# Kernel optimization log

Hardware: AMD Instinct MI355X
Metric: run time of the kernel (lower is better)

The kernel has to match this reference:

```python
import jax, jax.numpy as jnp
import numpy as np

D_MODEL = 512
NUM_HEADS = 8
DEPTH = D_MODEL // NUM_HEADS


def setup_inputs() -> dict:
    key = jax.random.key(0)
    kx, kq, kk, kv, ko = jax.random.split(key, 5)
    scale = 1.0 / np.sqrt(D_MODEL)
    return {
        "x": jax.random.normal(kx, (4, 2048, D_MODEL), dtype=jnp.float32),
        "W_q": jax.random.normal(kq, (D_MODEL, D_MODEL), dtype=jnp.float32) * scale,
        "W_k": jax.random.normal(kk, (D_MODEL, D_MODEL), dtype=jnp.float32) * scale,
        "W_v": jax.random.normal(kv, (D_MODEL, D_MODEL), dtype=jnp.float32) * scale,
        "W_o": jax.random.normal(ko, (D_MODEL, D_MODEL), dtype=jnp.float32) * scale,
    }


def reference(x, W_q, W_k, W_v, W_o):
    B, S, _ = x.shape
    # nn.Linear with weight W: y = x @ W.T
    def split_heads(t):
        return t.reshape(B, S, NUM_HEADS, DEPTH).transpose(0, 2, 1, 3)  # [B,H,S,D]
    Q = split_heads(x @ W_q.T)
    K = split_heads(x @ W_k.T)
    V = split_heads(x @ W_v.T)
    b = -jnp.log(jnp.asarray(S, dtype=jnp.float32))  # -log(seq_len) bias
    inv_sqrt_dk = 1.0 / jnp.sqrt(jnp.asarray(DEPTH, dtype=jnp.float32))
    qk = jnp.einsum('bhqd,bhkd->bhqk', Q, K) * inv_sqrt_dk
    attn = jax.nn.sigmoid(qk + b)  # non-softmax sigmoid attention
    out = jnp.einsum('bhqk,bhkd->bhqd', attn, V)
    out = out.transpose(0, 2, 1, 3).reshape(B, S, D_MODEL)
    return out @ W_o.T
```

## Files before the change

kernel.cpp:

```cpp
#include <hip/hip_runtime.h>
#include <stdint.h>

typedef _Float16 f16x8 __attribute__((ext_vector_type(8)));
typedef _Float16 f16x4 __attribute__((ext_vector_type(4)));
typedef __fp16 h16x2 __attribute__((ext_vector_type(2)));
typedef float f32x4 __attribute__((ext_vector_type(4)));
typedef float f32x16 __attribute__((ext_vector_type(16)));

#define SEQ 2048
#define NHEADS 8

#define GLOAD_LDS16(gp, lp)                                                        \
  __builtin_amdgcn_global_load_lds(                                                \
      (const __attribute__((address_space(1))) void*)(uintptr_t)(const void*)(gp), \
      (__attribute__((address_space(3))) void*)(uintptr_t)(void*)(lp), 16, 0, 0)

__device__ __forceinline__ void barrier_lds() {
  __builtin_amdgcn_s_waitcnt(0xc07f);
  __builtin_amdgcn_s_barrier();
}

__device__ __forceinline__ f16x4 pack4(float a, float b, float c, float d) {
  h16x2 lo = __builtin_amdgcn_cvt_pkrtz(a, b);
  h16x2 hi = __builtin_amdgcn_cvt_pkrtz(c, d);
  f16x4 o;
  o.x = (_Float16)lo.x; o.y = (_Float16)lo.y;
  o.z = (_Float16)hi.x; o.w = (_Float16)hi.y;
  return o;
}

__global__ void cvt_all_kernel(const float* __restrict__ x, const float* __restrict__ wq,
                               const float* __restrict__ wk, const float* __restrict__ wv,
                               const float* __restrict__ wo, _Float16* __restrict__ xh,
                               _Float16* __restrict__ wh) {
  int i = blockIdx.x * 256 + threadIdx.x;
  const float* src;
  _Float16* dst;
  int off;
  if (i < 1048576) {
    src = x; dst = xh; off = i;
  } else {
    int j = i - 1048576;
    int sel = j >> 16;
    off = j & 65535;
    src = (sel == 0) ? wq : (sel == 1) ? wk : (sel == 2) ? wv : wo;
    dst = wh + (size_t)sel * 262144;
  }
  float4 v = ((const float4*)src)[off];
  ((f16x4*)dst)[off] = pack4(v.x, v.y, v.z, v.w);
}

__device__ __forceinline__ void gemm_tile_bt(const _Float16* __restrict__ A,
                                             const _Float16* __restrict__ B,
                                             int m0, int n0,
                                             _Float16* lds,
                                             f32x4 (&acc)[4][4]) {
  const int tid = threadIdx.x;
  const int w = tid >> 6, lane = tid & 63;
  const int wr = w >> 1, wc = w & 1;
  const int lrow = lane & 15, q = lane >> 4;
  const int snb = w * 32 + (lane >> 3);
  const int scb = lane & 7;

#pragma unroll
  for (int i = 0; i < 4; ++i)
#pragma unroll
    for (int j = 0; j < 4; ++j)
#pragma unroll
      for (int r = 0; r < 4; ++r) acc[i][j][r] = 0.f;

#pragma unroll
  for (int t = 0; t < 4; ++t) {
    int n = snb + t * 8;
    int cbg = scb ^ (n & 7);
    GLOAD_LDS16(A + (size_t)(m0 + n) * 512 + cbg * 8, lds + (w * 32 + t * 8) * 64);
    GLOAD_LDS16(B + (size_t)(n0 + n) * 512 + cbg * 8, lds + 8192 + (w * 32 + t * 8) * 64);
  }

  for (int kt = 0; kt < 8; ++kt) {
    __syncthreads();
    if (kt < 7) {
      _Float16* nb = lds + ((kt + 1) & 1) * 16384;
#pragma unroll
      for (int t = 0; t < 4; ++t) {
        int n = snb + t * 8;
        int cbg = scb ^ (n & 7);
        GLOAD_LDS16(A + (size_t)(m0 + n) * 512 + (kt + 1) * 64 + cbg * 8, nb + (w * 32 + t * 8) * 64);
        GLOAD_LDS16(B + (size_t)(n0 + n) * 512 + (kt + 1) * 64 + cbg * 8, nb + 8192 + (w * 32 + t * 8) * 64);
      }
    }
    _Float16* As = lds + (kt & 1) * 16384;
    _Float16* Bs = As + 8192;

    f16x8 af[4][2], bfr[4][2];
#pragma unroll
    for (int i = 0; i < 4; ++i) {
      int m = wr * 64 + i * 16 + lrow;
#pragma unroll
      for (int kk = 0; kk < 2; ++kk) {
        int cb = (kk * 4 + q) ^ (m & 7);
        af[i][kk] = *(const f16x8*)(As + m * 64 + cb * 8);
      }
    }
#pragma unroll
    for (int j = 0; j < 4; ++j) {
      int n = wc * 64 + j * 16 + lrow;
#pragma unroll
      for (int kk = 0; kk < 2; ++kk) {
        int cb = (kk * 4 + q) ^ (n & 7);
        bfr[j][kk] = *(const f16x8*)(Bs + n * 64 + cb * 8);
      }
    }
#pragma unroll
    for (int i = 0; i < 4; ++i)
#pragma unroll
      for (int j = 0; j < 4; ++j) {
        acc[i][j] = __builtin_amdgcn_mfma_f32_16x16x32_f16(af[i][0], bfr[j][0], acc[i][j], 0, 0, 0);
        acc[i][j] = __builtin_amdgcn_mfma_f32_16x16x32_f16(af[i][1], bfr[j][1], acc[i][j], 0, 0, 0);
      }
  }
}

__global__ __launch_bounds__(256, 2) void qkv_kernel(
    const _Float16* __restrict__ xb, const _Float16* __restrict__ Wq,
    const _Float16* __restrict__ Wk, const _Float16* __restrict__ Wv,
    _Float16* __restrict__ Qo, _Float16* __restrict__ Ko, _Float16* __restrict__ Vto) {
  __shared__ _Float16 pool[32768];
  const int z = blockIdx.z;
  f32x4 acc[4][4];
  const int tid = threadIdx.x, w = tid >> 6, lane = tid & 63;
  const int wr = w >> 1, wc = w & 1, lcol = lane & 15, q = lane >> 4;

  if (z < 2) {
    const int m0 = blockIdx.y * 128;
    const int n0 = blockIdx.x * 128;
    gemm_tile_bt((z == 0) ? Wq : Wk, xb, m0, n0, pool, acc);
    _Float16* outp = (z == 0) ? Qo : Ko;
    __syncthreads();
#pragma unroll
    for (int i = 0; i < 4; ++i) {
      int cl = wr * 64 + i * 16 + q * 4;
#pragma unroll
      for (int j = 0; j < 4; ++j) {
        int s = wc * 64 + j * 16 + lcol;
        *(f16x4*)(pool + s * 136 + cl) =
            pack4(acc[i][j][0], acc[i][j][1], acc[i][j][2], acc[i][j][3]);
      }
    }
    __syncthreads();
#pragma unroll
    for (int it = 0; it < 16; ++it) {
      int srow = it * 8 + (tid >> 5);
      int ch = tid & 31;
      f16x4 v = *(const f16x4*)(pool + srow * 136 + ch * 4);
      *(f16x4*)(outp + (size_t)(n0 + srow) * 512 + m0 + ch * 4) = v;
    }
  } else {
    const int m0 = blockIdx.x * 128;
    const int n0 = blockIdx.y * 128;
    gemm_tile_bt(xb, Wv, m0, n0, pool, acc);
    const int bb = m0 >> 11, sl0 = m0 & 2047;
    __syncthreads();
#pragma unroll
    for (int i = 0; i < 4; ++i) {
      int s0 = wr * 64 + i * 16 + q * 4;
#pragma unroll
      for (int j = 0; j < 4; ++j) {
        int c = wc * 64 + j * 16 + lcol;
        *(f16x4*)(pool + c * 136 + s0) =
            pack4(acc[i][j][0], acc[i][j][1], acc[i][j][2], acc[i][j][3]);
      }
    }
    __syncthreads();
#pragma unroll
    for (int it = 0; it < 16; ++it) {
      int crow = it * 8 + (tid >> 5);
      int ch = tid & 31;
      int cg = n0 + crow, h = cg >> 6, d = cg & 63;
      f16x4 v = *(const f16x4*)(pool + crow * 136 + ch * 4);
      *(f16x4*)(Vto + ((size_t)((bb * NHEADS + h) * 64 + d)) * SEQ + sl0 + ch * 4) = v;
    }
  }
}

__device__ __forceinline__ void load_win(const _Float16* Ksc, const _Float16* Vtsc,
                                         int m, int klp, int hi, int q31,
                                         f16x8 (&ka)[4], f16x8 (&vb)[2][2]) {
  const int krow = m * 32 + klp;
#pragma unroll
  for (int s = 0; s < 4; ++s) {
    int cb = (s * 2 + hi) ^ (krow & 7);
    ka[s] = *(const f16x8*)(Ksc + krow * 64 + cb * 8);
  }
#pragma unroll
  for (int ww = 0; ww < 2; ++ww)
#pragma unroll
    for (int t = 0; t < 2; ++t) {
      int drow = t * 32 + q31;
      int g = m * 4 + ww * 2 + hi;
      int cb = g ^ (drow & 15);
      vb[ww][t] = *(const f16x8*)(Vtsc + drow * 128 + cb * 8);
    }
}

__device__ __forceinline__ void attn_window(const f16x8 (&ka)[4], const f16x8 (&vb)[2][2],
                                            const f16x8 (&qb)[4], const f32x16& z16,
                                            f32x16& o0, f32x16& o1) {
  const float c1 = 0.18033688011112042f;
  __builtin_amdgcn_s_setprio(1);
  f32x16 sacc = __builtin_amdgcn_mfma_f32_32x32x16_f16(ka[0], qb[0], z16, 0, 0, 0);
  sacc = __builtin_amdgcn_mfma_f32_32x32x16_f16(ka[1], qb[1], sacc, 0, 0, 0);
  sacc = __builtin_amdgcn_mfma_f32_32x32x16_f16(ka[2], qb[2], sacc, 0, 0, 0);
  sacc = __builtin_amdgcn_mfma_f32_32x32x16_f16(ka[3], qb[3], sacc, 0, 0, 0);
  __builtin_amdgcn_s_setprio(0);

  float p[16];
#pragma unroll
  for (int r = 0; r < 16; ++r) {
    float wp = __builtin_amdgcn_exp2f(__builtin_fmaf(sacc[r], c1, -1.0f));
    float e = wp * 0.0009765625f;
    p[r] = __builtin_fmaf(wp, __builtin_fmaf(e, e, -e), wp);
  }

  f16x8 pa[2];
#pragma unroll
  for (int ww = 0; ww < 2; ++ww) {
    h16x2 a0 = __builtin_amdgcn_cvt_pkrtz(p[8 * ww + 0], p[8 * ww + 1]);
    h16x2 a1 = __builtin_amdgcn_cvt_pkrtz(p[8 * ww + 2], p[8 * ww + 3]);
    h16x2 a2 = __builtin_amdgcn_cvt_pkrtz(p[8 * ww + 4], p[8 * ww + 5]);
    h16x2 a3 = __builtin_amdgcn_cvt_pkrtz(p[8 * ww + 6], p[8 * ww + 7]);
    pa[ww][0] = (_Float16)a0.x; pa[ww][1] = (_Float16)a0.y;
    pa[ww][2] = (_Float16)a1.x; pa[ww][3] = (_Float16)a1.y;
    pa[ww][4] = (_Float16)a2.x; pa[ww][5] = (_Float16)a2.y;
    pa[ww][6] = (_Float16)a3.x; pa[ww][7] = (_Float16)a3.y;
  }

  __builtin_amdgcn_s_setprio(1);
  o0 = __builtin_amdgcn_mfma_f32_32x32x16_f16(pa[0], vb[0][0], o0, 0, 0, 0);
  o1 = __builtin_amdgcn_mfma_f32_32x32x16_f16(pa[0], vb[0][1], o1, 0, 0, 0);
  o0 = __builtin_amdgcn_mfma_f32_32x32x16_f16(pa[1], vb[1][0], o0, 0, 0, 0);
  o1 = __builtin_amdgcn_mfma_f32_32x32x16_f16(pa[1], vb[1][1], o1, 0, 0, 0);
  __builtin_amdgcn_s_setprio(0);
}

__global__ __launch_bounds__(256, 2) void attn_kernel(
    const _Float16* __restrict__ Qw, const _Float16* __restrict__ Kw,
    const _Float16* __restrict__ Vtw, _Float16* __restrict__ Ow) {
  __shared__ _Float16 lds[32768];

  const int tid = threadIdx.x, w = tid >> 6, lane = tid & 63;
  const int q31 = lane & 31, hi = lane >> 5;

  const int L = blockIdx.x;
  const int xcd = L & 7, slot = L >> 3;
  const int bh = xcd * 4 + (slot >> 4), qt = slot & 15;
  const int b = bh >> 3, h = bh & 7;
  const int q0 = qt * 128;

  const _Float16* Qp = Qw + ((size_t)(b * SEQ + q0)) * 512 + h * 64;
  const _Float16* Kp = Kw + ((size_t)b * SEQ) * 512 + h * 64;
  const _Float16* Vp = Vtw + (size_t)bh * 64 * SEQ;

  const int snb = w * 32 + (lane >> 3), scb = lane & 7;
  const int vnb = w * 16 + (lane >> 4), vcb = lane & 15;

  int koff[4], voff[4];
  const int kcb = scb ^ (snb & 7);
#pragma unroll
  for (int t = 0; t < 4; ++t) {
    koff[t] = snb * 1024 + t * 8192 + kcb * 16;
    int nv = vnb + t * 4;
    voff[t] = nv * 4096 + (vcb ^ (nv & 15)) * 16;
  }
  const char* kgb = (const char*)Kp;
  const char* vgb = (const char*)Vp;

  _Float16* Qs = lds + 16384;
#pragma unroll
  for (int t = 0; t < 4; ++t) GLOAD_LDS16((const char*)Qp + koff[t], Qs + (w * 32 + t * 8) * 64);
#pragma unroll
  for (int t = 0; t < 4; ++t) GLOAD_LDS16(kgb + koff[t], lds + (w * 32 + t * 8) * 64);
#pragma unroll
  for (int t = 0; t < 4; ++t) GLOAD_LDS16(vgb + voff[t], lds + 8192 + (w * 16 + t * 4) * 128);
  kgb += 131072;
  vgb += 256;
  __syncthreads();

  f16x8 qb[4];
  const int qrow = w * 32 + q31;
#pragma unroll
  for (int s = 0; s < 4; ++s) {
    int cb = (s * 2 + hi) ^ (qrow & 7);
    qb[s] = *(const f16x8*)(Qs + qrow * 64 + cb * 8);
  }

  f32x16 oacc[2];
  f32x16 z16;
#pragma unroll
  for (int r = 0; r < 16; ++r) { z16[r] = 0.f; oacc[0][r] = 0.f; oacc[1][r] = 0.f; }

  const int klp = (q31 & 3) | ((q31 & 4) << 1) | ((q31 & 8) >> 1) | (q31 & 16);

  for (int kt = 0; kt < 16; ++kt) {
    __syncthreads();
    if (kt < 15) {
      _Float16* nb = lds + ((kt + 1) & 1) * 16384;
#pragma unroll
      for (int t = 0; t < 4; ++t) GLOAD_LDS16(kgb + koff[t], nb + (w * 32 + t * 8) * 64);
#pragma unroll
      for (int t = 0; t < 4; ++t) GLOAD_LDS16(vgb + voff[t], nb + 8192 + (w * 16 + t * 4) * 128);
      kgb += 131072;
      vgb += 256;
    }
    const _Float16* Ksc = lds + (kt & 1) * 16384;
    const _Float16* Vtsc = Ksc + 8192;

    f16x8 kaA[4], kaB[4], vbA[2][2], vbB[2][2];
    load_win(Ksc, Vtsc, 0, klp, hi, q31, kaA, vbA);
    load_win(Ksc, Vtsc, 1, klp, hi, q31, kaB, vbB);
    attn_window(kaA, vbA, qb, z16, oacc[0], oacc[1]);
    load_win(Ksc, Vtsc, 2, klp, hi, q31, kaA, vbA);
    attn_window(kaB, vbB, qb, z16, oacc[0], oacc[1]);
    load_win(Ksc, Vtsc, 3, klp, hi, q31, kaB, vbB);
    attn_window(kaA, vbA, qb, z16, oacc[0], oacc[1]);
    attn_window(kaB, vbB, qb, z16, oacc[0], oacc[1]);
  }

  barrier_lds();
  _Float16* Ob = lds;
#pragma unroll
  for (int t = 0; t < 2; ++t) {
#pragma unroll
    for (int r = 0; r < 16; ++r) {
      int row = w * 32 + (r & 3) + ((r >> 2) << 3) + hi * 4;
      int d = t * 32 + q31;
      Ob[row * 72 + d] = (_Float16)(oacc[t][r] * 0.0009765625f);
    }
  }
  barrier_lds();
#pragma unroll
  for (int it = 0; it < 8; ++it) {
    int row = it * 16 + (tid >> 4);
    int ch = tid & 15;
    f16x4 v = *(const f16x4*)(Ob + row * 72 + ch * 4);
    *(f16x4*)(Ow + (size_t)(b * SEQ + q0 + row) * 512 + h * 64 + ch * 4) = v;
  }
}

__global__ __launch_bounds__(256, 2) void oproj_kernel(
    const _Float16* __restrict__ A, const _Float16* __restrict__ Wo,
    float* __restrict__ out) {
  __shared__ _Float16 pool[32768];
  const int m0 = blockIdx.x * 128, n0 = blockIdx.y * 128;
  f32x4 acc[4][4];
  gemm_tile_bt(A, Wo, m0, n0, pool, acc);

  const int tid = threadIdx.x, w = tid >> 6, lane = tid & 63;
  const int wr = w >> 1, wc = w & 1, lcol = lane & 15, q = lane >> 4;
#pragma unroll
  for (int i = 0; i < 4; ++i) {
    int gm0 = m0 + wr * 64 + i * 16 + q * 4;
#pragma unroll
    for (int j = 0; j < 4; ++j) {
      int gn = n0 + wc * 64 + j * 16 + lcol;
#pragma unroll
      for (int r = 0; r < 4; ++r)
        out[(size_t)(gm0 + r) * 512 + gn] = acc[i][j][r];
    }
  }
}

extern "C" void kernel_launch(void* const* d_in, const int* in_sizes, int n_in,
                              void* d_out, int out_size, void* d_ws, size_t ws_size,
                              hipStream_t stream) {
  const float* x = (const float*)d_in[0];
  const float* Wq = (const float*)d_in[1];
  const float* Wk = (const float*)d_in[2];
  const float* Wv = (const float*)d_in[3];
  const float* Wo = (const float*)d_in[4];
  float* out = (float*)d_out;
  char* ws = (char*)d_ws;

  _Float16* xh = (_Float16*)(ws + 0);
  _Float16* wh = (_Float16*)(ws + 8388608);
  _Float16* Qw = (_Float16*)(ws + 10485760);
  _Float16* Kw = (_Float16*)(ws + 18874368);
  _Float16* Vtw = (_Float16*)(ws + 27262976);
  _Float16* Ow = (_Float16*)(ws + 35651584);

  _Float16* wqh = wh;
  _Float16* wkh = wh + 262144;
  _Float16* wvh = wh + 524288;
  _Float16* woh = wh + 786432;

  cvt_all_kernel<<<5120, 256, 0, stream>>>(x, Wq, Wk, Wv, Wo, xh, wh);
  qkv_kernel<<<dim3(64, 4, 3), 256, 0, stream>>>(xh, wqh, wkh, wvh, Qw, Kw, Vtw);
  attn_kernel<<<512, 256, 0, stream>>>(Qw, Kw, Vtw, Ow);
  oproj_kernel<<<dim3(64, 4), 256, 0, stream>>>(Ow, woh, out);
}
```

Baseline: 153.9 us.

## Split attention key range across two blocks and combine partial outputs

```diff
diff --git a/kernel.cpp b/kernel.cpp
--- a/kernel.cpp
+++ b/kernel.cpp
@@ -184,12 +184,13 @@
 }
 
 __device__ __forceinline__ void load_win(const _Float16* Ksc, const _Float16* Vtsc,
-                                         int m, int klp, int hi, int q31,
+                                         int m, int klp, int fk, int fq,
+                                         int hi, int q31,
                                          f16x8 (&ka)[4], f16x8 (&vb)[2][2]) {
   const int krow = m * 32 + klp;
 #pragma unroll
   for (int s = 0; s < 4; ++s) {
-    int cb = (s * 2 + hi) ^ (krow & 7);
+    int cb = (s * 2 + hi) ^ fk;
     ka[s] = *(const f16x8*)(Ksc + krow * 64 + cb * 8);
   }
 #pragma unroll
@@ -198,8 +199,8 @@
     for (int t = 0; t < 2; ++t) {
       int drow = t * 32 + q31;
       int g = m * 4 + ww * 2 + hi;
-      int cb = g ^ (drow & 15);
-      vb[ww][t] = *(const f16x8*)(Vtsc + drow * 128 + cb * 8);
+      int cb = g ^ fq;
+      vb[ww][t] = *(const f16x8*)(Vtsc + drow * 64 + cb * 8);
     }
 }
 
@@ -243,54 +244,65 @@
   __builtin_amdgcn_s_setprio(0);
 }
 
-__global__ __launch_bounds__(256, 2) void attn_kernel(
+__global__ __launch_bounds__(256, 4) void attn_kernel(
     const _Float16* __restrict__ Qw, const _Float16* __restrict__ Kw,
-    const _Float16* __restrict__ Vtw, _Float16* __restrict__ Ow) {
-  __shared__ _Float16 lds[32768];
+    const _Float16* __restrict__ Vtw, _Float16* __restrict__ Ow,
+    _Float16* __restrict__ Op) {
+  __shared__ _Float16 lds[16384];
 
   const int tid = threadIdx.x, w = tid >> 6, lane = tid & 63;
   const int q31 = lane & 31, hi = lane >> 5;
 
   const int L = blockIdx.x;
   const int xcd = L & 7, slot = L >> 3;
-  const int bh = xcd * 4 + (slot >> 4), qt = slot & 15;
+  const int bh = xcd * 4 + (slot >> 5);
+  const int rem = slot & 31;
+  const int qt = rem >> 1, ks = rem & 1;
   const int b = bh >> 3, h = bh & 7;
   const int q0 = qt * 128;
 
   const _Float16* Qp = Qw + ((size_t)(b * SEQ + q0)) * 512 + h * 64;
-  const _Float16* Kp = Kw + ((size_t)b * SEQ) * 512 + h * 64;
-  const _Float16* Vp = Vtw + (size_t)bh * 64 * SEQ;
-
-  const int snb = w * 32 + (lane >> 3), scb = lane & 7;
-  const int vnb = w * 16 + (lane >> 4), vcb = lane & 15;
-
-  int koff[4], voff[4];
-  const int kcb = scb ^ (snb & 7);
-#pragma unroll
-  for (int t = 0; t < 4; ++t) {
-    koff[t] = snb * 1024 + t * 8192 + kcb * 16;
-    int nv = vnb + t * 4;
-    voff[t] = nv * 4096 + (vcb ^ (nv & 15)) * 16;
+  const _Float16* Kp = Kw + ((size_t)b * SEQ) * 512 + h * 64 + (size_t)ks * 1024 * 512;
+  const _Float16* Vp = Vtw + (size_t)bh * 64 * SEQ + (size_t)ks * 1024;
+
+  const int l3 = lane >> 3, l7 = lane & 7;
+
+  int koff[2], voff[2];
+#pragma unroll
+  for (int t = 0; t < 2; ++t) {
+    int n = w * 16 + t * 8 + l3;
+    int cbg = l7 ^ l3 ^ ((t & 1) << 2);
+    koff[t] = n * 1024 + cbg * 16;
+    voff[t] = n * 4096 + cbg * 16;
   }
   const char* kgb = (const char*)Kp;
   const char* vgb = (const char*)Vp;
 
-  _Float16* Qs = lds + 16384;
-#pragma unroll
-  for (int t = 0; t < 4; ++t) GLOAD_LDS16((const char*)Qp + koff[t], Qs + (w * 32 + t * 8) * 64);
-#pragma unroll
-  for (int t = 0; t < 4; ++t) GLOAD_LDS16(kgb + koff[t], lds + (w * 32 + t * 8) * 64);
-#pragma unroll
-  for (int t = 0; t < 4; ++t) GLOAD_LDS16(vgb + voff[t], lds + 8192 + (w * 16 + t * 4) * 128);
-  kgb += 131072;
-  vgb += 256;
+  _Float16* Qs = lds + 8192;
+#pragma unroll
+  for (int t = 0; t < 4; ++t) {
+    int n = w * 32 + t * 8 + l3;
+    int cbg = l7 ^ l3 ^ ((t & 1) << 2);
+    GLOAD_LDS16((const char*)Qp + n * 1024 + cbg * 16, Qs + (w * 32 + t * 8) * 64);
+  }
+#pragma unroll
+  for (int t = 0; t < 2; ++t) {
+    GLOAD_LDS16(kgb + koff[t], lds + (w * 16 + t * 8) * 64);
+    GLOAD_LDS16(vgb + voff[t], lds + 4096 + (w * 16 + t * 8) * 64);
+  }
+  kgb += 65536;
+  vgb += 128;
   __syncthreads();
+
+  const int fq = (q31 & 7) ^ (((q31 >> 3) & 1) << 2);
+  const int klp = (q31 & 3) | ((q31 & 4) << 1) | ((q31 & 8) >> 1) | (q31 & 16);
+  const int fk = (klp & 7) ^ (((klp >> 3) & 1) << 2);
 
   f16x8 qb[4];
   const int qrow = w * 32 + q31;
 #pragma unroll
   for (int s = 0; s < 4; ++s) {
-    int cb = (s * 2 + hi) ^ (qrow & 7);
+    int cb = (s * 2 + hi) ^ fq;
     qb[s] = *(const f16x8*)(Qs + qrow * 64 + cb * 8);
   }
 
@@ -299,35 +311,31 @@
 #pragma unroll
   for (int r = 0; r < 16; ++r) { z16[r] = 0.f; oacc[0][r] = 0.f; oacc[1][r] = 0.f; }
 
-  const int klp = (q31 & 3) | ((q31 & 4) << 1) | ((q31 & 8) >> 1) | (q31 & 16);
-
   for (int kt = 0; kt < 16; ++kt) {
     __syncthreads();
     if (kt < 15) {
-      _Float16* nb = lds + ((kt + 1) & 1) * 16384;
-#pragma unroll
-      for (int t = 0; t < 4; ++t) GLOAD_LDS16(kgb + koff[t], nb + (w * 32 + t * 8) * 64);
-#pragma unroll
-      for (int t = 0; t < 4; ++t) GLOAD_LDS16(vgb + voff[t], nb + 8192 + (w * 16 + t * 4) * 128);
-      kgb += 131072;
-      vgb += 256;
-    }
-    const _Float16* Ksc = lds + (kt & 1) * 16384;
-    const _Float16* Vtsc = Ksc + 8192;
-
-    f16x8 kaA[4], kaB[4], vbA[2][2], vbB[2][2];
-    load_win(Ksc, Vtsc, 0, klp, hi, q31, kaA, vbA);
-    load_win(Ksc, Vtsc, 1, klp, hi, q31, kaB, vbB);
-    attn_window(kaA, vbA, qb, z16, oacc[0], oacc[1]);
-    load_win(Ksc, Vtsc, 2, klp, hi, q31, kaA, vbA);
-    attn_window(kaB, vbB, qb, z16, oacc[0], oacc[1]);
-    load_win(Ksc, Vtsc, 3, klp, hi, q31, kaB, vbB);
-    attn_window(kaA, vbA, qb, z16, oacc[0], oacc[1]);
-    attn_window(kaB, vbB, qb, z16, oacc[0], oacc[1]);
+      _Float16* nb = lds + ((kt + 1) & 1) * 8192;
+#pragma unroll
+      for (int t = 0; t < 2; ++t) {
+        GLOAD_LDS16(kgb + koff[t], nb + (w * 16 + t * 8) * 64);
+        GLOAD_LDS16(vgb + voff[t], nb + 4096 + (w * 16 + t * 8) * 64);
+      }
+      kgb += 65536;
+      vgb += 128;
+    }
+    const _Float16* Ksc = lds + (kt & 1) * 8192;
+    const _Float16* Vtsc = Ksc + 4096;
+
+    f16x8 ka0[4], ka1[4], vb0[2][2], vb1[2][2];
+    load_win(Ksc, Vtsc, 0, klp, fk, fq, hi, q31, ka0, vb0);
+    attn_window(ka0, vb0, qb, z16, oacc[0], oacc[1]);
+    load_win(Ksc, Vtsc, 1, klp, fk, fq, hi, q31, ka1, vb1);
+    attn_window(ka1, vb1, qb, z16, oacc[0], oacc[1]);
   }
 
   barrier_lds();
   _Float16* Ob = lds;
+  _Float16* outp = ks ? Op : Ow;
 #pragma unroll
   for (int t = 0; t < 2; ++t) {
 #pragma unroll
@@ -343,8 +351,15 @@
     int row = it * 16 + (tid >> 4);
     int ch = tid & 15;
     f16x4 v = *(const f16x4*)(Ob + row * 72 + ch * 4);
-    *(f16x4*)(Ow + (size_t)(b * SEQ + q0 + row) * 512 + h * 64 + ch * 4) = v;
-  }
+    *(f16x4*)(outp + (size_t)(b * SEQ + q0 + row) * 512 + h * 64 + ch * 4) = v;
+  }
+}
+
+__global__ void combine_kernel(_Float16* __restrict__ o, const _Float16* __restrict__ p) {
+  int i = blockIdx.x * 256 + threadIdx.x;
+  f16x8 a = ((const f16x8*)o)[i];
+  f16x8 c = ((const f16x8*)p)[i];
+  ((f16x8*)o)[i] = a + c;
 }
 
 __global__ __launch_bounds__(256, 2) void oproj_kernel(
@@ -395,6 +410,7 @@
 
   cvt_all_kernel<<<5120, 256, 0, stream>>>(x, Wq, Wk, Wv, Wo, xh, wh);
   qkv_kernel<<<dim3(64, 4, 3), 256, 0, stream>>>(xh, wqh, wkh, wvh, Qw, Kw, Vtw);
-  attn_kernel<<<512, 256, 0, stream>>>(Qw, Kw, Vtw, Ow);
+  attn_kernel<<<1024, 256, 0, stream>>>(Qw, Kw, Vtw, Ow, xh);
+  combine_kernel<<<2048, 256, 0, stream>>>(Ow, xh);
   oproj_kernel<<<dim3(64, 4), 256, 0, stream>>>(Ow, woh, out);
 }
```

Result: slower. 161.9 us (+5.1%).
